# Performance work log

Measured on AMD Instinct MI355X. Metric: run time of the kernel, lower is better.

The kernel has to match this reference:

```python
import jax, jax.numpy as jnp
import numpy as np

N, D = 8192, 1024
Q = 4096
DK = 512
DV = 256


def setup_inputs() -> dict:
    key = jax.random.key(0)
    k1, k2, k3, k4, k5, k6 = jax.random.split(key, 6)
    return {
        "search_x": jax.random.normal(k1, (N, D), dtype=jnp.float32),
        "search_y": jax.random.normal(k2, (N, DV), dtype=jnp.float32),
        "query_x": jax.random.normal(k3, (Q, D), dtype=jnp.float32),
        "mask": jax.random.randint(k4, (Q, N), 0, 2, dtype=jnp.int64),
        "Wk": jax.random.normal(k5, (D, DK), dtype=jnp.float32) / np.sqrt(D),
        "Wq": jax.random.normal(k6, (D, DK), dtype=jnp.float32) / np.sqrt(D),
    }


def reference(search_x, search_y, query_x, mask, Wk, Wq):
    # key/query modules: bias-free linear projections (n_keys == 1 after _ensure_key_shape)
    keys = search_x @ Wk            # [N, DK]
    qk = query_x @ Wq               # [Q, DK]
    scale = 1.0 / jnp.sqrt(jnp.asarray(DK, dtype=keys.dtype))
    logits = (qk @ keys.T) * scale  # [Q, N]  (== broadcast mul+sum in original)
    # masked softmax over the search dimension (dim=1)
    m = mask > 0                    # [Q, N]
    neg = jnp.finfo(logits.dtype).min
    p = jax.nn.softmax(jnp.where(m, logits, neg), axis=1)
    p = jnp.where(m, p, 0.0)
    # values = noop_value_module(search_x, search_y) = search_y  [N, DV]
    res = p @ search_y              # [Q, DV]
    return res[:, None, :]          # [Q, n_keys=1, DV], matching original output shape
```

## Files before the change

kernel.cpp:

```cpp
#include <hip/hip_runtime.h>
#include <hip/hip_fp16.h>

typedef _Float16 half4v __attribute__((ext_vector_type(4)));
typedef _Float16 half8v __attribute__((ext_vector_type(8)));
typedef float floatx4 __attribute__((ext_vector_type(4)));

#define GLOBAL_AS __attribute__((address_space(1)))
#define LDS_AS __attribute__((address_space(3)))

__device__ __forceinline__ void async_copy16(const _Float16* g, _Float16* l) {
    __builtin_amdgcn_global_load_lds((const GLOBAL_AS unsigned int*)g,
                                     (LDS_AS unsigned int*)l, 16, 0, 0);
}

__device__ __forceinline__ void transpose_tile(const float* __restrict__ in,
                                               _Float16* __restrict__ out,
                                               int R, int C, int bx, int by,
                                               float* tile ) {
    int tx = threadIdx.x & 31, ty = threadIdx.x >> 5;
    int bc = bx * 32, br = by * 32;
#pragma unroll
    for (int i = 0; i < 32; i += 8)
        tile[(ty + i) * 33 + tx] = in[(size_t)(br + ty + i) * C + bc + tx];
    __syncthreads();
#pragma unroll
    for (int i = 0; i < 32; i += 8)
        out[(size_t)(bc + ty + i) * R + br + tx] = (_Float16)tile[tx * 33 + ty + i];
}

__global__ __launch_bounds__(256) void k_preproc(const float* __restrict__ x,
                                                 _Float16* __restrict__ xh,
                                                 const float* __restrict__ q,
                                                 _Float16* __restrict__ qh,
                                                 const float* __restrict__ Wk,
                                                 _Float16* __restrict__ wkT,
                                                 const float* __restrict__ Wq,
                                                 _Float16* __restrict__ wqT,
                                                 const float* __restrict__ y,
                                                 _Float16* __restrict__ yT) {
    __shared__ float tile[32 * 33];
    const int b = blockIdx.x;
    if (b < 12288) {
        const int na = 8192 * 1024;
        int i = (b * 256 + threadIdx.x) * 4;
        const float* src;
        _Float16* dst;
        if (i < na) { src = x + i; dst = xh + i; }
        else        { src = q + (i - na); dst = qh + (i - na); }
        float4 v = *(const float4*)src;
        half4v h;
        h[0] = (_Float16)v.x; h[1] = (_Float16)v.y;
        h[2] = (_Float16)v.z; h[3] = (_Float16)v.w;
        *(half4v*)dst = h;
    } else if (b < 12800) {
        const int idx = b - 12288;
        transpose_tile(Wk, wkT, 1024, 512, idx & 15, idx >> 4, tile);
    } else if (b < 13312) {
        const int idx = b - 12800;
        transpose_tile(Wq, wqT, 1024, 512, idx & 15, idx >> 4, tile);
    } else {
        const int idx = b - 13312;
        transpose_tile(y, yT, 8192, 256, idx & 7, idx >> 3, tile);
    }
}

template <int OUT_MODE>
__global__ __launch_bounds__(256) void k_gemm_nt(const _Float16* __restrict__ A,
                                                 const _Float16* __restrict__ B,
                                                 void* __restrict__ C,
                                                 const _Float16* __restrict__ A2,
                                                 const _Float16* __restrict__ B2,
                                                 void* __restrict__ C2,
                                                 int M, int N, int K, int kChunk,
                                                 float scale, float scale2) {
    __shared__ __align__(16) _Float16 As[128 * 64];
    __shared__ __align__(16) _Float16 Bs[128 * 64];
    const int tid  = threadIdx.x;
    const int lane = tid & 63;
    const int wave = tid >> 6;
    const int wm   = (wave >> 1) * 64;
    const int wn   = (wave & 1) * 64;
    const int quad = lane >> 4;
    const int lr   = lane & 15;

    int by = blockIdx.y;
    if (OUT_MODE == 3 && by >= 64) {
        by -= 64;
        A = A2; B = B2; C = C2; scale = scale2;
    }
    const long m0 = (long)by * 128;
    const long n0 = (long)blockIdx.x * 128;
    const int kBegin = blockIdx.z * kChunk;
    const int kEnd   = kBegin + kChunk;

    floatx4 acc[4][4] = {};

    const int rl = lane >> 3;
    const int gc = (lane & 7) ^ rl;
    const long arow = m0 + wave * 32 + rl;
    const long brow = n0 + wave * 32 + rl;

    for (int kt = kBegin; kt < kEnd; kt += 64) {
        const _Float16* Ap = A + arow * (long)K + kt + gc * 8;
        const _Float16* Bp = B + brow * (long)K + kt + gc * 8;
        _Float16* Al = &As[(wave * 32) * 64];
        _Float16* Bl = &Bs[(wave * 32) * 64];
#pragma unroll
        for (int i = 0; i < 4; ++i) {
            async_copy16(Ap + (long)(i * 8) * K, Al + i * 8 * 64);
            async_copy16(Bp + (long)(i * 8) * K, Bl + i * 8 * 64);
        }
        __syncthreads();

#pragma unroll
        for (int kk = 0; kk < 64; kk += 32) {
            half8v af[4], bf[4];
            const int cg = (kk >> 3) + quad;
            const int sl = (cg ^ (lr & 7)) * 8;
#pragma unroll
            for (int i = 0; i < 4; ++i)
                af[i] = *(const half8v*)&As[(wm + i * 16 + lr) * 64 + sl];
#pragma unroll
            for (int j = 0; j < 4; ++j)
                bf[j] = *(const half8v*)&Bs[(wn + j * 16 + lr) * 64 + sl];
#pragma unroll
            for (int i = 0; i < 4; ++i)
#pragma unroll
                for (int j = 0; j < 4; ++j)
                    acc[i][j] = __builtin_amdgcn_mfma_f32_16x16x32_f16(af[i], bf[j], acc[i][j], 0, 0, 0);
        }
        __syncthreads();
    }

#pragma unroll
    for (int i = 0; i < 4; ++i) {
        long rbase = m0 + wm + i * 16 + quad * 4;
#pragma unroll
        for (int j = 0; j < 4; ++j) {
            long col = n0 + wn + j * 16 + lr;
#pragma unroll
            for (int r = 0; r < 4; ++r) {
                float val = acc[i][j][r] * scale;
                if (OUT_MODE == 1)
                    ((float*)C)[(size_t)blockIdx.z * M * N + (rbase + r) * (long)N + col] = val;
                else
                    ((_Float16*)C)[(rbase + r) * (long)N + col] = (_Float16)val;
            }
        }
    }
}

template <int Z>
__global__ __launch_bounds__(256) void k_reduce(const float* __restrict__ part,
                                                float* __restrict__ out, int n) {
    int i = (blockIdx.x * 256 + threadIdx.x) * 4;
    if (i >= n) return;
    float4 s = *(const float4*)(part + i);
#pragma unroll
    for (int z = 1; z < Z; ++z) {
        float4 v = *(const float4*)(part + (size_t)z * n + i);
        s.x += v.x; s.y += v.y; s.z += v.z; s.w += v.w;
    }
    *(float4*)(out + i) = s;
}

__global__ __launch_bounds__(256) void k_softmax(_Float16* __restrict__ logits,
                                                 const int* __restrict__ mask) {
    const int q   = blockIdx.x;
    const int tid = threadIdx.x;
    _Float16* row   = logits + (size_t)q * 8192;
    const int* mrow = mask + (size_t)q * 8192;

    float v[32];
    unsigned mb = 0;
    float lmax = -3.0e38f;
#pragma unroll
    for (int i = 0; i < 8; ++i) {
        int base = i * 1024 + tid * 4;
        int4 mm  = *(const int4*)(mrow + base);
        half4v h = *(const half4v*)(row + base);
#pragma unroll
        for (int j = 0; j < 4; ++j) v[i * 4 + j] = (float)h[j];
        if (mm.x > 0) { mb |= 1u << (i * 4 + 0); lmax = fmaxf(lmax, v[i * 4 + 0]); }
        if (mm.y > 0) { mb |= 1u << (i * 4 + 1); lmax = fmaxf(lmax, v[i * 4 + 1]); }
        if (mm.z > 0) { mb |= 1u << (i * 4 + 2); lmax = fmaxf(lmax, v[i * 4 + 2]); }
        if (mm.w > 0) { mb |= 1u << (i * 4 + 3); lmax = fmaxf(lmax, v[i * 4 + 3]); }
    }
#pragma unroll
    for (int off = 32; off > 0; off >>= 1) lmax = fmaxf(lmax, __shfl_xor(lmax, off, 64));
    __shared__ float redmax[4], redsum[4];
    if ((tid & 63) == 0) redmax[tid >> 6] = lmax;
    __syncthreads();
    lmax = fmaxf(fmaxf(redmax[0], redmax[1]), fmaxf(redmax[2], redmax[3]));

    float lsum = 0.f;
#pragma unroll
    for (int i = 0; i < 32; ++i) {
        float e = ((mb >> i) & 1u) ? __expf(v[i] - lmax) : 0.f;
        v[i] = e;
        lsum += e;
    }
#pragma unroll
    for (int off = 32; off > 0; off >>= 1) lsum += __shfl_xor(lsum, off, 64);
    if ((tid & 63) == 0) redsum[tid >> 6] = lsum;
    __syncthreads();
    lsum = redsum[0] + redsum[1] + redsum[2] + redsum[3];
    float inv = lsum > 0.f ? 1.f / lsum : 0.f;

#pragma unroll
    for (int i = 0; i < 8; ++i) {
        int base = i * 1024 + tid * 4;
        half4v h;
#pragma unroll
        for (int j = 0; j < 4; ++j) h[j] = (_Float16)(v[i * 4 + j] * inv);
        *(half4v*)(row + base) = h;
    }
}

extern "C" void kernel_launch(void* const* d_in, const int* in_sizes, int n_in,
                              void* d_out, int out_size, void* d_ws, size_t ws_size,
                              hipStream_t stream) {
    const float* search_x = (const float*)d_in[0];
    const float* search_y = (const float*)d_in[1];
    const float* query_x  = (const float*)d_in[2];
    const int*   mask     = (const int*)d_in[3];
    const float* Wk       = (const float*)d_in[4];
    const float* Wq       = (const float*)d_in[5];
    (void)in_sizes; (void)n_in; (void)ws_size; (void)out_size;

    char* p = (char*)d_ws;
    _Float16* xh   = (_Float16*)p; p += (size_t)8192 * 1024 * 2;
    _Float16* qh   = (_Float16*)p; p += (size_t)4096 * 1024 * 2;
    _Float16* wkT  = (_Float16*)p; p += (size_t)512 * 1024 * 2;
    _Float16* wqT  = (_Float16*)p; p += (size_t)512 * 1024 * 2;
    _Float16* yT   = (_Float16*)p; p += (size_t)256 * 8192 * 2;
    _Float16* keys = (_Float16*)p; p += (size_t)8192 * 512 * 2;
    _Float16* qk   = (_Float16*)p; p += (size_t)4096 * 512 * 2;
    _Float16* lg   = (_Float16*)p; p += (size_t)4096 * 8192 * 2;
    float*    part = (float*)p;    p += (size_t)4 * 4096 * 256 * 4;

    k_preproc<<<15360, 256, 0, stream>>>(search_x, xh, query_x, qh,
                                         Wk, wkT, Wq, wqT, search_y, yT);

    k_gemm_nt<3><<<dim3(4, 96, 1), 256, 0, stream>>>(
        xh, wkT, keys, qh, wqT, qk, 8192, 512, 1024, 1024,
        1.0f, 0.04419417382415922f);

    k_gemm_nt<0><<<dim3(64, 32, 1), 256, 0, stream>>>(
        qk, keys, lg, nullptr, nullptr, nullptr, 4096, 8192, 512, 512, 1.0f, 0.f);

    k_softmax<<<4096, 256, 0, stream>>>(lg, mask);

    k_gemm_nt<1><<<dim3(2, 32, 4), 256, 0, stream>>>(
        lg, yT, part, nullptr, nullptr, nullptr, 4096, 256, 8192, 2048, 1.0f, 0.f);
    k_reduce<4><<<1024, 256, 0, stream>>>(part, (float*)d_out, 4096 * 256);
}
```

Baseline: 352.5 us.

## Replace logits GEMM with 256x256-tile 8-wave pipelined kernel

```diff
diff --git a/kernel.cpp b/kernel.cpp
--- a/kernel.cpp
+++ b/kernel.cpp
@@ -150,6 +150,135 @@
     }
 }
 
+#define UNROLL _Pragma("unroll")
+
+#define LOAD_AF(QA)                                                            \
+    UNROLL for (int fi = 0; fi < 4; ++fi)                                      \
+    UNROLL for (int s = 0; s < 2; ++s)                                         \
+        af[fi][s] = *(const half8v*)&As[buf][((QA) * 128 + wm * 64 + fi * 16 + lr) * 64 + \
+                                            (((s * 4 + quad) ^ (lr & 7)) * 8)];
+
+#define LOAD_BF(DST, QB)                                                       \
+    UNROLL for (int fj = 0; fj < 2; ++fj)                                      \
+    UNROLL for (int s = 0; s < 2; ++s)                                         \
+        DST[fj][s] = *(const half8v*)&Bs[buf][((QB) * 128 + wn * 32 + fj * 16 + lr) * 64 + \
+                                             (((s * 4 + quad) ^ (lr & 7)) * 8)];
+
+#define MFMA_Q(QA, QB, BF)                                                     \
+    __builtin_amdgcn_s_setprio(1);                                             \
+    UNROLL for (int fi = 0; fi < 4; ++fi)                                      \
+    UNROLL for (int fj = 0; fj < 2; ++fj)                                      \
+    UNROLL for (int s = 0; s < 2; ++s)                                         \
+        acc[QA][fi][QB][fj] = __builtin_amdgcn_mfma_f32_16x16x32_f16(          \
+            af[fi][s], (BF)[fj][s], acc[QA][fi][QB][fj], 0, 0, 0);             \
+    __builtin_amdgcn_s_setprio(0);
+
+#define BAR()                                                                  \
+    __builtin_amdgcn_s_barrier();                                              \
+    __builtin_amdgcn_sched_barrier(0);
+
+__global__ __launch_bounds__(512, 2) void k_gemm_8p(const _Float16* __restrict__ A,
+                                                    const _Float16* __restrict__ B,
+                                                    _Float16* __restrict__ C,
+                                                    int M, int N, int K) {
+    __shared__ __align__(16) _Float16 As[2][256 * 64];
+    __shared__ __align__(16) _Float16 Bs[2][256 * 64];
+    const int tid  = threadIdx.x;
+    const int lane = tid & 63;
+    const int wave = tid >> 6;
+    const int wm   = wave >> 2;
+    const int wn   = wave & 3;
+    const int quad = lane >> 4;
+    const int lr   = lane & 15;
+    const long m0 = (long)blockIdx.y * 256;
+    const long n0 = (long)blockIdx.x * 256;
+
+    const int gchunk = (tid & 7) ^ ((tid >> 3) & 7);
+    auto stage_half = [&](const _Float16* __restrict__ G, _Float16* __restrict__ Sb,
+                          long r0, int h, int kt) {
+#pragma unroll
+        for (int c = 0; c < 2; ++c) {
+            const int rb = h * 128 + c * 64;
+            const _Float16* g = G + (r0 + rb + (tid >> 3)) * (long)K + kt + gchunk * 8;
+            async_copy16(g, Sb + (rb + wave * 8) * 64);
+        }
+    };
+
+    floatx4 acc[2][4][2][2] = {};
+    half8v af[4][2], bf0[2][2], bf1[2][2];
+
+    const int NT = K / 64;
+    stage_half(A, &As[0][0], m0, 0, 0);
+    stage_half(B, &Bs[0][0], n0, 0, 0);
+    stage_half(B, &Bs[0][0], n0, 1, 0);
+    stage_half(A, &As[0][0], m0, 1, 0);
+
+    int buf = 0;
+    for (int t = 0; t < NT - 1; ++t) {
+        const int nb = buf ^ 1;
+        const int ktn = (t + 1) * 64;
+        _Float16* Anext = &As[nb][0];
+        _Float16* Bnext = &Bs[nb][0];
+        stage_half(A, Anext, m0, 0, ktn);
+        asm volatile("s_waitcnt vmcnt(6)" ::: "memory");
+        BAR();
+        LOAD_AF(0);
+        LOAD_BF(bf0, 0);
+        MFMA_Q(0, 0, bf0);
+        BAR();
+        stage_half(B, Bnext, n0, 0, ktn);
+        asm volatile("s_waitcnt vmcnt(6)" ::: "memory");
+        BAR();
+        LOAD_BF(bf1, 1);
+        MFMA_Q(0, 1, bf1);
+        BAR();
+        stage_half(B, Bnext, n0, 1, ktn);
+        asm volatile("s_waitcnt vmcnt(6)" ::: "memory");
+        BAR();
+        LOAD_AF(1);
+        MFMA_Q(1, 0, bf0);
+        BAR();
+        stage_half(A, Anext, m0, 1, ktn);
+        BAR();
+        MFMA_Q(1, 1, bf1);
+        BAR();
+        buf = nb;
+    }
+    asm volatile("s_waitcnt vmcnt(4)" ::: "memory");
+    BAR();
+    LOAD_AF(0);
+    LOAD_BF(bf0, 0);
+    MFMA_Q(0, 0, bf0);
+    BAR();
+    asm volatile("s_waitcnt vmcnt(2)" ::: "memory");
+    BAR();
+    LOAD_BF(bf1, 1);
+    MFMA_Q(0, 1, bf1);
+    BAR();
+    asm volatile("s_waitcnt vmcnt(0)" ::: "memory");
+    BAR();
+    LOAD_AF(1);
+    MFMA_Q(1, 0, bf0);
+    BAR();
+    MFMA_Q(1, 1, bf1);
+
+#pragma unroll
+    for (int qa = 0; qa < 2; ++qa)
+#pragma unroll
+    for (int fi = 0; fi < 4; ++fi) {
+        const long rbase = m0 + qa * 128 + wm * 64 + fi * 16 + quad * 4;
+#pragma unroll
+        for (int qb = 0; qb < 2; ++qb)
+#pragma unroll
+        for (int fj = 0; fj < 2; ++fj) {
+            const long col = n0 + qb * 128 + wn * 32 + fj * 16 + lr;
+#pragma unroll
+            for (int r = 0; r < 4; ++r)
+                C[(rbase + r) * (long)N + col] = (_Float16)acc[qa][fi][qb][fj][r];
+        }
+    }
+}
+
 template <int Z>
 __global__ __launch_bounds__(256) void k_reduce(const float* __restrict__ part,
                                                 float* __restrict__ out, int n) {
@@ -246,8 +375,7 @@
         xh, wkT, keys, qh, wqT, qk, 8192, 512, 1024, 1024,
         1.0f, 0.04419417382415922f);
 
-    k_gemm_nt<0><<<dim3(64, 32, 1), 256, 0, stream>>>(
-        qk, keys, lg, nullptr, nullptr, nullptr, 4096, 8192, 512, 512, 1.0f, 0.f);
+    k_gemm_8p<<<dim3(32, 16), 512, 0, stream>>>(qk, keys, lg, 4096, 8192, 512);
 
     k_softmax<<<4096, 256, 0, stream>>>(lg, mask);
 
```

Result: no change. 358.6 us (+1.7%).
